# Performance work log

Hardware: AMD Instinct MI355X
Metric: run time of the kernel (lower is better)

Reference implementation:

```python
import jax, jax.numpy as jnp
import numpy as np

B, S, H, D, V = 256, 128, 1024, 256, 1858


def setup_inputs() -> dict:
    key = jax.random.key(0)
    ks = jax.random.split(key, 13)
    s = 1.0 / np.sqrt(H)
    return {
        "hidden_states": jax.random.normal(ks[0], (B, S, H), jnp.float32),
        "Wf": jax.random.normal(ks[1], (D, H), jnp.float32) * s,
        "bf": jax.random.normal(ks[2], (D,), jnp.float32) * 0.01,
        "Wt": jax.random.normal(ks[3], (D, H), jnp.float32) * s,
        "bt": jax.random.normal(ks[4], (D,), jnp.float32) * 0.01,
        "Wg": jax.random.normal(ks[5], (D, H), jnp.float32) * s,
        "bg": jax.random.normal(ks[6], (D,), jnp.float32) * 0.01,
        "promo_tab": jax.random.normal(ks[7], (5, D), jnp.float32),
        "Ws": jax.random.normal(ks[8], (1, D), jnp.float32) * (1.0 / np.sqrt(D)),
        "bs": jax.random.normal(ks[9], (1,), jnp.float32) * 0.01,
        "from_sqs": jax.random.randint(ks[10], (V,), 0, 64, jnp.int32),
        "to_sqs": jax.random.randint(ks[11], (V,), 0, 64, jnp.int32),
        "promo_types": jax.random.randint(ks[12], (V,), 0, 5, jnp.int32),
    }


def reference(hidden_states, Wf, bf, Wt, bt, Wg, bg, promo_tab, Ws, bs,
              from_sqs, to_sqs, promo_types):
    # hidden_states: [B, S, H]; squares are tokens 3:67, global token is 0.
    sq_hidden = hidden_states[:, 3:67, :]          # [B, 64, H]
    global_hidden = hidden_states[:, 0, :]         # [B, H]

    # Linear commutes with gather: project the 64 unique squares first,
    # then gather per move (same math as gather-then-project).
    fp = jnp.einsum('bsh,dh->bsd', sq_hidden, Wf) + bf   # [B, 64, D]
    tp = jnp.einsum('bsh,dh->bsd', sq_hidden, Wt) + bt   # [B, 64, D]
    gp = global_hidden @ Wg.T + bg                       # [B, D]

    from_proj = fp[:, from_sqs, :]                       # [B, V, D]
    to_proj = tp[:, to_sqs, :]                           # [B, V, D]
    promo_feats = promo_tab[promo_types]                 # [V, D]

    combined = from_proj * to_proj + gp[:, None, :] + promo_feats[None]
    # score_proj: Linear(D, 1), then squeeze(-1) -> [B, V]
    return jnp.einsum('bvd,d->bv', jax.nn.relu(combined), Ws[0]) + bs[0]
```

## Files before the change

kernel.cpp:

```cpp
#include <hip/hip_runtime.h>

#define NB   256
#define NSQ  64
#define NH   1024
#define ND   256
#define NV   1858
#define M_   (NB * NSQ)
#define N_   512
#define K_   1024

typedef __attribute__((ext_vector_type(4))) float f32x4;
typedef __attribute__((ext_vector_type(8))) short bf16x8;

__device__ __forceinline__ unsigned short bf16_rne(float x) {
    unsigned u = __float_as_uint(x);
    unsigned r = u + 0x7fffu + ((u >> 16) & 1u);
    return (unsigned short)(r >> 16);
}

__device__ __forceinline__ void gload16(const void* g, void* l) {
    __builtin_amdgcn_global_load_lds(
        (const __attribute__((address_space(1))) unsigned int*)g,
        (__attribute__((address_space(3))) unsigned int*)l, 16, 0, 0);
}

__global__ __launch_bounds__(256) void cast_kernel(
    const float* __restrict__ hid,
    const float* __restrict__ Wf, const float* __restrict__ Wt,
    unsigned short* __restrict__ Ahi, unsigned short* __restrict__ Alo,
    unsigned short* __restrict__ Whi, unsigned short* __restrict__ Wlo) {
    int bidx = blockIdx.x;
    if (bidx < 16384) {
        int idx = bidx * 256 + threadIdx.x;
        int m = idx >> 8;
        int q = idx & 255;
        int b = m >> 6, s = m & 63;
        const float4* src = (const float4*)(hid + (size_t)(b * 128 + 3 + s) * NH);
        float4 v = src[q];
        float vv[4] = {v.x, v.y, v.z, v.w};
        unsigned short hh[4], ll[4];
#pragma unroll
        for (int j = 0; j < 4; ++j) {
            hh[j] = bf16_rne(vv[j]);
            float hf = __uint_as_float((unsigned)hh[j] << 16);
            ll[j] = bf16_rne(vv[j] - hf);
        }
        ((ushort4*)Ahi)[idx] = make_ushort4(hh[0], hh[1], hh[2], hh[3]);
        ((ushort4*)Alo)[idx] = make_ushort4(ll[0], ll[1], ll[2], ll[3]);
    } else {
        int idx = (bidx - 16384) * 256 + threadIdx.x;
        int n = idx >> 8, q = idx & 255;
        const float* srow = (n < ND) ? (Wf + (size_t)n * NH) : (Wt + (size_t)(n - ND) * NH);
        float4 v = ((const float4*)srow)[q];
        float vv[4] = {v.x, v.y, v.z, v.w};
        unsigned short hh[4], ll[4];
#pragma unroll
        for (int j = 0; j < 4; ++j) {
            hh[j] = bf16_rne(vv[j]);
            float hf = __uint_as_float((unsigned)hh[j] << 16);
            ll[j] = bf16_rne(vv[j] - hf);
        }
        ((ushort4*)Whi)[idx] = make_ushort4(hh[0], hh[1], hh[2], hh[3]);
        ((ushort4*)Wlo)[idx] = make_ushort4(ll[0], ll[1], ll[2], ll[3]);
    }
}

__global__ __launch_bounds__(1024) void gp_kernel(
    const float* __restrict__ hid, const float* __restrict__ Wg,
    const float* __restrict__ bg, float* __restrict__ gp) {
    __shared__ float h[NH];
    int b = blockIdx.x;
    int tid = threadIdx.x;
    if (tid < 256) ((float4*)h)[tid] = ((const float4*)(hid + (size_t)b * 128 * NH))[tid];
    __syncthreads();
    int wave = tid >> 6, lane = tid & 63;
    const float4* hs = (const float4*)h;
    for (int dd = 0; dd < 16; ++dd) {
        int d = wave * 16 + dd;
        const float4* wrow = (const float4*)(Wg + (size_t)d * NH);
        float acc = 0.f;
#pragma unroll
        for (int p = 0; p < 4; ++p) {
            float4 w = wrow[p * 64 + lane];
            float4 x = hs[p * 64 + lane];
            acc += w.x * x.x + w.y * x.y + w.z * x.z + w.w * x.w;
        }
#pragma unroll
        for (int o = 32; o > 0; o >>= 1) acc += __shfl_xor(acc, o, 64);
        if (lane == 0) gp[(size_t)b * ND + d] = acc + bg[d];
    }
}

__global__ __launch_bounds__(256) void gemm3_kernel(
    const unsigned short* __restrict__ Ahi, const unsigned short* __restrict__ Alo,
    const unsigned short* __restrict__ Whi, const unsigned short* __restrict__ Wlo,
    const float* __restrict__ bfv, const float* __restrict__ btv,
    float* __restrict__ C) {
    __shared__ unsigned short lAh[128 * 32], lAl[128 * 32];
    __shared__ unsigned short lBh[128 * 32], lBl[128 * 32];
    int tid = threadIdx.x;
    int bid = blockIdx.x;
    int nt = bid & 3;
    int mt = bid >> 2;
    const unsigned short* gAh = Ahi + (size_t)mt * 128 * K_;
    const unsigned short* gAl = Alo + (size_t)mt * 128 * K_;
    const unsigned short* gBh = Whi + (size_t)nt * 128 * K_;
    const unsigned short* gBl = Wlo + (size_t)nt * 128 * K_;
    int lane = tid & 63, wv = tid >> 6;
    int wm = (wv >> 1) * 64, wn = (wv & 1) * 64;
    int fr = lane & 15, kh = lane >> 4;
    f32x4 acc[4][4] = {};

    for (int kt = 0; kt < K_; kt += 32) {
#pragma unroll
        for (int is = 0; is < 2; ++is) {
            int o = is * 4096 + tid * 16;
            int r = o >> 6;
            int c = (o & 63) >> 1;
            size_t ge = (size_t)r * K_ + kt + c;
            gload16(gAh + ge, (char*)lAh + o);
            gload16(gAl + ge, (char*)lAl + o);
            gload16(gBh + ge, (char*)lBh + o);
            gload16(gBl + ge, (char*)lBl + o);
        }
        __syncthreads();
        bf16x8 ah[4], al[4], bh[4], bl[4];
#pragma unroll
        for (int f = 0; f < 4; ++f) {
            int ea = (wm + f * 16 + fr) * 32 + kh * 8;
            int eb = (wn + f * 16 + fr) * 32 + kh * 8;
            ah[f] = *(const bf16x8*)&lAh[ea];
            al[f] = *(const bf16x8*)&lAl[ea];
            bh[f] = *(const bf16x8*)&lBh[eb];
            bl[f] = *(const bf16x8*)&lBl[eb];
        }
#pragma unroll
        for (int i = 0; i < 4; ++i)
#pragma unroll
            for (int j = 0; j < 4; ++j) {
                acc[i][j] = __builtin_amdgcn_mfma_f32_16x16x32_bf16(ah[i], bh[j], acc[i][j], 0, 0, 0);
                acc[i][j] = __builtin_amdgcn_mfma_f32_16x16x32_bf16(ah[i], bl[j], acc[i][j], 0, 0, 0);
                acc[i][j] = __builtin_amdgcn_mfma_f32_16x16x32_bf16(al[i], bh[j], acc[i][j], 0, 0, 0);
            }
        __syncthreads();
    }

    const float* bias = (nt < 2) ? bfv : btv;
    int nb0 = nt * 128 - ((nt < 2) ? 0 : 256);
#pragma unroll
    for (int j = 0; j < 4; ++j) {
        int ncol = nt * 128 + wn + j * 16 + fr;
        float bv = bias[nb0 + wn + j * 16 + fr];
#pragma unroll
        for (int i = 0; i < 4; ++i) {
            int mrow = mt * 128 + wm + i * 16 + kh * 4;
#pragma unroll
            for (int r = 0; r < 4; ++r) {
                C[(size_t)(mrow + r) * N_ + ncol] = acc[i][j][r] + bv;
            }
        }
    }
}

__global__ __launch_bounds__(1024) void out_kernel(
    const float* __restrict__ C, const float* __restrict__ gp,
    const float* __restrict__ promo_tab, const float* __restrict__ Wsv,
    const float* __restrict__ bsv,
    const int* __restrict__ from_sqs, const int* __restrict__ to_sqs,
    const int* __restrict__ ptypes, float* __restrict__ out) {
    __shared__ float cb[NSQ * N_];
    __shared__ float gpl[ND];
    __shared__ float wsl[ND];
    __shared__ float pl[5 * ND];
    __shared__ int fsq[NV], tsq[NV], pty[NV];
    int b = blockIdx.x;
    int tid = threadIdx.x;
    const float4* src = (const float4*)(C + (size_t)b * NSQ * N_);
    float4* dst = (float4*)cb;
#pragma unroll
    for (int i = 0; i < 8; ++i) dst[tid + i * 1024] = src[tid + i * 1024];
    if (tid < 64) ((float4*)gpl)[tid] = ((const float4*)(gp + (size_t)b * ND))[tid];
    else if (tid < 128) ((float4*)wsl)[tid - 64] = ((const float4*)Wsv)[tid - 64];
    else if (tid < 448) ((float4*)pl)[tid - 128] = ((const float4*)promo_tab)[tid - 128];
    for (int v = tid; v < NV; v += 1024) {
        fsq[v] = from_sqs[v];
        tsq[v] = to_sqs[v];
        pty[v] = ptypes[v];
    }
    __syncthreads();

    int wave = tid >> 6, lane = tid & 63;
    float bias0 = bsv[0];
    const float4* cb4 = (const float4*)cb;
    const float4* gp4 = (const float4*)gpl;
    const float4* ws4 = (const float4*)wsl;
    const float4* pl4 = (const float4*)pl;
    for (int v = wave; v < NV; v += 16) {
        int sf = fsq[v];
        int st = tsq[v];
        int p  = pty[v];
        float4 a = cb4[sf * 128 + lane];
        float4 t = cb4[st * 128 + 64 + lane];
        float4 g = gp4[lane];
        float4 pp = pl4[p * 64 + lane];
        float4 w = ws4[lane];
        float c0 = a.x * t.x + g.x + pp.x;
        float c1 = a.y * t.y + g.y + pp.y;
        float c2 = a.z * t.z + g.z + pp.z;
        float c3 = a.w * t.w + g.w + pp.w;
        float s = fmaxf(c0, 0.f) * w.x + fmaxf(c1, 0.f) * w.y +
                  fmaxf(c2, 0.f) * w.z + fmaxf(c3, 0.f) * w.w;
#pragma unroll
        for (int o = 32; o > 0; o >>= 1) s += __shfl_xor(s, o, 64);
        if (lane == 0) out[(size_t)b * NV + v] = s + bias0;
    }
}

extern "C" void kernel_launch(void* const* d_in, const int* in_sizes, int n_in,
                              void* d_out, int out_size, void* d_ws, size_t ws_size,
                              hipStream_t stream) {
    (void)in_sizes; (void)n_in; (void)out_size; (void)ws_size;
    const float* hid   = (const float*)d_in[0];
    const float* Wf    = (const float*)d_in[1];
    const float* bfv   = (const float*)d_in[2];
    const float* Wt    = (const float*)d_in[3];
    const float* btv   = (const float*)d_in[4];
    const float* Wg    = (const float*)d_in[5];
    const float* bgv   = (const float*)d_in[6];
    const float* promo = (const float*)d_in[7];
    const float* Wsv   = (const float*)d_in[8];
    const float* bsv   = (const float*)d_in[9];
    const int* from_sqs = (const int*)d_in[10];
    const int* to_sqs   = (const int*)d_in[11];
    const int* ptypes   = (const int*)d_in[12];
    float* out = (float*)d_out;

    char* ws = (char*)d_ws;
    unsigned short* Ahi = (unsigned short*)(ws);
    unsigned short* Alo = (unsigned short*)(ws + 33554432);
    unsigned short* Whi = (unsigned short*)(ws + 67108864);
    unsigned short* Wlo = (unsigned short*)(ws + 68157440);
    float* C  = (float*)(ws + 69206016);
    float* gp = (float*)(ws + 102760448);

    cast_kernel<<<16896, 256, 0, stream>>>(hid, Wf, Wt, Ahi, Alo, Whi, Wlo);
    gp_kernel<<<256, 1024, 0, stream>>>(hid, Wg, bgv, gp);
    gemm3_kernel<<<512, 256, 0, stream>>>(Ahi, Alo, Whi, Wlo, bfv, btv, C);
    out_kernel<<<256, 1024, 0, stream>>>(C, gp, promo, Wsv, bsv,
                                         from_sqs, to_sqs, ptypes, out);
}
```

Measured before the change: 330.1 us.

## Pre-tile bf16 split operands into contiguous LDS-ready blocks and remap GEMM workgroups

The cast kernel now writes the hi/lo bf16 operands in a tiled layout where each 128x32 K-slice is one contiguous 8 KB chunk, arranged so the GEMM's LDS fragment reads use a conflict-reduced pattern (kh*128 + fr*8). The GEMM loads each tile with fully contiguous global_load_lds transfers instead of strided row reads. Workgroup IDs are also permuted so consecutive blocks spread across XCDs. The cast kernel handles 8 elements per thread with 16-byte stores. The cost is a more complex index mapping that both kernels must agree on.

```diff
diff --git a/kernel.cpp b/kernel.cpp
--- a/kernel.cpp
+++ b/kernel.cpp
@@ -8,9 +8,11 @@
 #define M_   (NB * NSQ)
 #define N_   512
 #define K_   1024
+#define NKT  32
 
 typedef __attribute__((ext_vector_type(4))) float f32x4;
 typedef __attribute__((ext_vector_type(8))) short bf16x8;
+typedef __attribute__((ext_vector_type(8))) unsigned short u16x8;
 
 __device__ __forceinline__ unsigned short bf16_rne(float x) {
     unsigned u = __float_as_uint(x);
@@ -27,42 +29,49 @@
 __global__ __launch_bounds__(256) void cast_kernel(
     const float* __restrict__ hid,
     const float* __restrict__ Wf, const float* __restrict__ Wt,
-    unsigned short* __restrict__ Ahi, unsigned short* __restrict__ Alo,
-    unsigned short* __restrict__ Whi, unsigned short* __restrict__ Wlo) {
-    int bidx = blockIdx.x;
-    if (bidx < 16384) {
-        int idx = bidx * 256 + threadIdx.x;
-        int m = idx >> 8;
-        int q = idx & 255;
-        int b = m >> 6, s = m & 63;
-        const float4* src = (const float4*)(hid + (size_t)(b * 128 + 3 + s) * NH);
-        float4 v = src[q];
-        float vv[4] = {v.x, v.y, v.z, v.w};
-        unsigned short hh[4], ll[4];
-#pragma unroll
-        for (int j = 0; j < 4; ++j) {
-            hh[j] = bf16_rne(vv[j]);
-            float hf = __uint_as_float((unsigned)hh[j] << 16);
-            ll[j] = bf16_rne(vv[j] - hf);
-        }
-        ((ushort4*)Ahi)[idx] = make_ushort4(hh[0], hh[1], hh[2], hh[3]);
-        ((ushort4*)Alo)[idx] = make_ushort4(ll[0], ll[1], ll[2], ll[3]);
+    char* __restrict__ Ahi, char* __restrict__ Alo,
+    char* __restrict__ Whi, char* __restrict__ Wlo) {
+    int bid = blockIdx.x;
+    int tid = threadIdx.x;
+    int o = tid * 16;
+    int g_l = o >> 10;
+    int w = o & 1023;
+    int s = w >> 8;
+    int r = (w >> 4) & 15;
+    const float* src;
+    char* dh; char* dl;
+    if (bid < 8192) {
+        int brow = bid >> 5;
+        int kt = bid & 31;
+        int m = brow * 64 + g_l * 16 + r;
+        int b = m >> 6, sr = m & 63;
+        int k = kt * 32 + s * 8;
+        src = hid + (size_t)(b * 128 + 3 + sr) * NH + k;
+        size_t outb = ((size_t)((brow >> 1) * 32 + kt) << 13) + ((brow & 1) << 12) + o;
+        dh = Ahi + outb; dl = Alo + outb;
     } else {
-        int idx = (bidx - 16384) * 256 + threadIdx.x;
-        int n = idx >> 8, q = idx & 255;
-        const float* srow = (n < ND) ? (Wf + (size_t)n * NH) : (Wt + (size_t)(n - ND) * NH);
-        float4 v = ((const float4*)srow)[q];
-        float vv[4] = {v.x, v.y, v.z, v.w};
-        unsigned short hh[4], ll[4];
-#pragma unroll
-        for (int j = 0; j < 4; ++j) {
-            hh[j] = bf16_rne(vv[j]);
-            float hf = __uint_as_float((unsigned)hh[j] << 16);
-            ll[j] = bf16_rne(vv[j] - hf);
-        }
-        ((ushort4*)Whi)[idx] = make_ushort4(hh[0], hh[1], hh[2], hh[3]);
-        ((ushort4*)Wlo)[idx] = make_ushort4(ll[0], ll[1], ll[2], ll[3]);
-    }
+        int bid2 = bid - 8192;
+        int nrb = bid2 >> 5;
+        int kt = bid2 & 31;
+        int n = nrb * 64 + g_l * 16 + r;
+        int k = kt * 32 + s * 8;
+        src = ((n < ND) ? (Wf + (size_t)n * NH) : (Wt + (size_t)(n - ND) * NH)) + k;
+        size_t outb = ((size_t)((nrb >> 1) * 32 + kt) << 13) + ((nrb & 1) << 12) + o;
+        dh = Whi + outb; dl = Wlo + outb;
+    }
+    float4 v0 = ((const float4*)src)[0];
+    float4 v1 = ((const float4*)src)[1];
+    float vv[8] = {v0.x, v0.y, v0.z, v0.w, v1.x, v1.y, v1.z, v1.w};
+    u16x8 h, l;
+#pragma unroll
+    for (int j = 0; j < 8; ++j) {
+        unsigned short hb = bf16_rne(vv[j]);
+        float hf = __uint_as_float((unsigned)hb << 16);
+        h[j] = hb;
+        l[j] = bf16_rne(vv[j] - hf);
+    }
+    *(u16x8*)dh = h;
+    *(u16x8*)dl = l;
 }
 
 __global__ __launch_bounds__(1024) void gp_kernel(
@@ -92,43 +101,38 @@
 }
 
 __global__ __launch_bounds__(256) void gemm3_kernel(
-    const unsigned short* __restrict__ Ahi, const unsigned short* __restrict__ Alo,
-    const unsigned short* __restrict__ Whi, const unsigned short* __restrict__ Wlo,
+    const char* __restrict__ Ahi, const char* __restrict__ Alo,
+    const char* __restrict__ Whi, const char* __restrict__ Wlo,
     const float* __restrict__ bfv, const float* __restrict__ btv,
     float* __restrict__ C) {
     __shared__ unsigned short lAh[128 * 32], lAl[128 * 32];
     __shared__ unsigned short lBh[128 * 32], lBl[128 * 32];
     int tid = threadIdx.x;
-    int bid = blockIdx.x;
-    int nt = bid & 3;
-    int mt = bid >> 2;
-    const unsigned short* gAh = Ahi + (size_t)mt * 128 * K_;
-    const unsigned short* gAl = Alo + (size_t)mt * 128 * K_;
-    const unsigned short* gBh = Whi + (size_t)nt * 128 * K_;
-    const unsigned short* gBl = Wlo + (size_t)nt * 128 * K_;
+    int wgid = (blockIdx.x & 7) * 64 + (blockIdx.x >> 3);
+    int nt = wgid & 3;
+    int mt = wgid >> 2;
     int lane = tid & 63, wv = tid >> 6;
     int wm = (wv >> 1) * 64, wn = (wv & 1) * 64;
     int fr = lane & 15, kh = lane >> 4;
     f32x4 acc[4][4] = {};
 
-    for (int kt = 0; kt < K_; kt += 32) {
+    for (int kt = 0; kt < NKT; ++kt) {
+        size_t ta = (size_t)(mt * NKT + kt) << 13;
+        size_t tb = (size_t)(nt * NKT + kt) << 13;
 #pragma unroll
         for (int is = 0; is < 2; ++is) {
             int o = is * 4096 + tid * 16;
-            int r = o >> 6;
-            int c = (o & 63) >> 1;
-            size_t ge = (size_t)r * K_ + kt + c;
-            gload16(gAh + ge, (char*)lAh + o);
-            gload16(gAl + ge, (char*)lAl + o);
-            gload16(gBh + ge, (char*)lBh + o);
-            gload16(gBl + ge, (char*)lBl + o);
+            gload16(Ahi + ta + o, (char*)lAh + o);
+            gload16(Alo + ta + o, (char*)lAl + o);
+            gload16(Whi + tb + o, (char*)lBh + o);
+            gload16(Wlo + tb + o, (char*)lBl + o);
         }
         __syncthreads();
         bf16x8 ah[4], al[4], bh[4], bl[4];
 #pragma unroll
         for (int f = 0; f < 4; ++f) {
-            int ea = (wm + f * 16 + fr) * 32 + kh * 8;
-            int eb = (wn + f * 16 + fr) * 32 + kh * 8;
+            int ea = (wm + f * 16) * 32 + kh * 128 + fr * 8;
+            int eb = (wn + f * 16) * 32 + kh * 128 + fr * 8;
             ah[f] = *(const bf16x8*)&lAh[ea];
             al[f] = *(const bf16x8*)&lAl[ea];
             bh[f] = *(const bf16x8*)&lBh[eb];
@@ -236,14 +240,14 @@
     float* out = (float*)d_out;
 
     char* ws = (char*)d_ws;
-    unsigned short* Ahi = (unsigned short*)(ws);
-    unsigned short* Alo = (unsigned short*)(ws + 33554432);
-    unsigned short* Whi = (unsigned short*)(ws + 67108864);
-    unsigned short* Wlo = (unsigned short*)(ws + 68157440);
+    char* Ahi = ws;
+    char* Alo = ws + 33554432;
+    char* Whi = ws + 67108864;
+    char* Wlo = ws + 68157440;
     float* C  = (float*)(ws + 69206016);
     float* gp = (float*)(ws + 102760448);
 
-    cast_kernel<<<16896, 256, 0, stream>>>(hid, Wf, Wt, Ahi, Alo, Whi, Wlo);
+    cast_kernel<<<8448, 256, 0, stream>>>(hid, Wf, Wt, Ahi, Alo, Whi, Wlo);
     gp_kernel<<<256, 1024, 0, stream>>>(hid, Wg, bgv, gp);
     gemm3_kernel<<<512, 256, 0, stream>>>(Ahi, Alo, Whi, Wlo, bfv, btv, C);
     out_kernel<<<256, 1024, 0, stream>>>(C, gp, promo, Wsv, bsv,
```

New measurement: 336.0 us. No clear change (+1.8%).
